# Performance work log

Measured on AMD Instinct MI355X. Metric: run time of the kernel, lower is better.

## Reference

```python
import jax, jax.numpy as jnp
import numpy as np

N, E, G = 40000, 640000, 32
H, HEADS, L, O = 128, 4, 4, 100
C = H // HEADS


def setup_inputs() -> dict:
    key = jax.random.key(0)
    ks = iter(jax.random.split(key, 40))
    def w(shape, fan):
        return jax.random.normal(next(ks), shape, jnp.float32) / np.float32(np.sqrt(fan))
    inp = {}
    inp["x"] = jax.random.normal(next(ks), (N, 4), jnp.float32)
    inp["edge_attr"] = jax.random.normal(next(ks), (E, 5), jnp.float32)
    inp["node_w"] = w((4, H), 4); inp["node_b"] = jnp.zeros((H,), jnp.float32)
    inp["edge_w"] = w((5, H), 5); inp["edge_b"] = jnp.zeros((H,), jnp.float32)
    inp["Wq"] = w((L, H, H), H); inp["bq"] = jnp.zeros((L, H), jnp.float32)
    inp["Wk"] = w((L, H, H), H); inp["bk"] = jnp.zeros((L, H), jnp.float32)
    inp["Wv"] = w((L, H, H), H); inp["bv"] = jnp.zeros((L, H), jnp.float32)
    inp["We"] = w((L, H, H), H)  # lin_edge has bias=False in PyG TransformerConv
    inp["Wskip"] = w((L, H, H), H); inp["bskip"] = jnp.zeros((L, H), jnp.float32)
    inp["ln_g"] = jnp.ones((L, H), jnp.float32); inp["ln_b"] = jnp.zeros((L, H), jnp.float32)
    inp["dos_w1"] = w((H, H // 2), H); inp["dos_b1"] = jnp.zeros((H // 2,), jnp.float32)
    inp["dos_w2"] = w((H // 2, O), H // 2); inp["dos_b2"] = jnp.zeros((O,), jnp.float32)
    inp["tr_w1"] = w((H, H // 2), H); inp["tr_b1"] = jnp.zeros((H // 2,), jnp.float32)
    inp["tr_w2"] = w((H // 2, O), H // 2); inp["tr_b2"] = jnp.zeros((O,), jnp.float32)
    inp["edge_index"] = jax.random.randint(next(ks), (2, E), 0, N, jnp.int32)
    inp["batch"] = jnp.sort(jax.random.randint(next(ks), (N,), 0, G, jnp.int32))
    return inp


def _seg_softmax(a, seg, n):
    # numerically stable scatter-softmax over edges grouped by destination node
    m = jax.ops.segment_max(a, seg, num_segments=n)
    e = jnp.exp(a - m[seg])
    s = jax.ops.segment_sum(e, seg, num_segments=n)
    return e / (s[seg] + 1e-16)


def _layer_norm(x, g, b, eps=1e-5):
    mu = x.mean(-1, keepdims=True)
    var = ((x - mu) ** 2).mean(-1, keepdims=True)
    return (x - mu) * jax.lax.rsqrt(var + eps) * g + b


def _forward(x, edge_attr, node_w, node_b, edge_w, edge_b, Wq, bq, Wk, bk, Wv, bv,
             We, Wskip, bskip, ln_g, ln_b,
             dos_w1, dos_b1, dos_w2, dos_b2, tr_w1, tr_b1, tr_w2, tr_b2,
             edge_index, batch):
    src, dst = edge_index[0], edge_index[1]  # PyG default flow: source->target
    n = x.shape[0]
    h = x @ node_w + node_b        # [N, H] node_proj
    e_h = edge_attr @ edge_w + edge_b  # [E, H] edge_proj (shared across layers)
    scale = np.float32(1.0 / np.sqrt(C))
    for i in range(L):  # TransformerConv -> LayerNorm -> ReLU (dropout is eval-mode no-op)
        q = (h @ Wq[i] + bq[i]).reshape(n, HEADS, C)
        k = (h @ Wk[i] + bk[i]).reshape(n, HEADS, C)
        v = (h @ Wv[i] + bv[i]).reshape(n, HEADS, C)
        e = (e_h @ We[i]).reshape(-1, HEADS, C)
        kj = k[src] + e            # [E, heads, C]
        vj = v[src] + e
        alpha = jnp.sum(q[dst] * kj, axis=-1) * scale  # [E, heads]
        alpha = _seg_softmax(alpha, dst, n)
        msg = vj * alpha[..., None]
        out = jax.ops.segment_sum(msg, dst, num_segments=n).reshape(n, H)
        out = out + h @ Wskip[i] + bskip[i]  # root_weight skip
        h = jax.nn.relu(_layer_norm(out, ln_g[i], ln_b[i]))
    # global mean pool per graph
    sums = jax.ops.segment_sum(h, batch, num_segments=G)
    cnt = jax.ops.segment_sum(jnp.ones((n, 1), h.dtype), batch, num_segments=G)
    hg = sums / jnp.maximum(cnt, 1.0)
    dos = jax.nn.relu(hg @ dos_w1 + dos_b1) @ dos_w2 + dos_b2
    tr = jax.nn.relu(hg @ tr_w1 + tr_b1) @ tr_w2 + tr_b2
    return dos, tr


def reference(x, edge_attr, node_w, node_b, edge_w, edge_b, Wq, bq, Wk, bk, Wv, bv,
              We, Wskip, bskip, ln_g, ln_b,
              dos_w1, dos_b1, dos_w2, dos_b2, tr_w1, tr_b1, tr_w2, tr_b2,
              edge_index, batch):
    return _forward(x, edge_attr, node_w, node_b, edge_w, edge_b, Wq, bq, Wk, bk, Wv, bv,
                    We, Wskip, bskip, ln_g, ln_b,
                    dos_w1, dos_b1, dos_w2, dos_b2, tr_w1, tr_b1, tr_w2, tr_b2,
                    edge_index, batch)
```

## Files before the change

kernel.cpp:

```cpp
#include <hip/hip_runtime.h>
#include <hip/hip_fp16.h>
#include <math.h>

#define N_NODES 40000
#define N_EDGES 640000
#define N_GRAPHS 32
#define HDIM 128
#define NHEADS 4
#define CDIM 32
#define NLAYERS 4
#define ODIM 100
#define SCAN_B 256
#define SCAN_NBLK ((N_NODES + SCAN_B - 1) / SCAN_B)
#define M_PAD 40064
#define POOL_CHUNK 32
#define POOL_NBLK ((N_NODES + POOL_CHUNK - 1) / POOL_CHUNK)
#define SCALE 0.17677669529663687f

typedef __bf16 bf16_t;
typedef bf16_t bf16x8 __attribute__((ext_vector_type(8)));
typedef float f32x4 __attribute__((ext_vector_type(4)));
typedef _Float16 h2v __attribute__((ext_vector_type(2)));

#if defined(__has_builtin)
#if __has_builtin(__builtin_amdgcn_fdot2)
#define HAVE_FDOT2 1
#endif
#endif

struct __align__(8) H2P { __half2 k; __half2 v; };

__global__ void nodeproj_kernel(const float* __restrict__ x,
                                const float* __restrict__ w,
                                const float* __restrict__ b,
                                bf16_t* __restrict__ hb) {
    int idx = blockIdx.x * blockDim.x + threadIdx.x;
    if (idx >= N_NODES * HDIM) return;
    int n = idx >> 7, c = idx & 127;
    float s = b[c];
    s += x[n * 4 + 0] * w[0 * HDIM + c];
    s += x[n * 4 + 1] * w[1 * HDIM + c];
    s += x[n * 4 + 2] * w[2 * HDIM + c];
    s += x[n * 4 + 3] * w[3 * HDIM + c];
    hb[idx] = (bf16_t)s;
}

__global__ void fold_edge_kernel(const float* __restrict__ edge_w,
                                 const float* __restrict__ edge_b,
                                 const float* __restrict__ We,
                                 float* __restrict__ Me_all,
                                 float* __restrict__ ce_all) {
    int blk = blockIdx.x;
    int i = blk / 6, j = blk % 6;
    int c = threadIdx.x;
    const float* W = We + (size_t)i * HDIM * HDIM;
    float s = 0.0f;
    if (j < 5) {
        for (int k = 0; k < HDIM; ++k) s += edge_w[j * HDIM + k] * W[k * HDIM + c];
        Me_all[i * 5 * HDIM + j * HDIM + c] = s;
    } else {
        for (int k = 0; k < HDIM; ++k) s += edge_b[k] * W[k * HDIM + c];
        ce_all[i * HDIM + c] = s;
    }
}

__global__ void count_deg_kernel(const int* __restrict__ ei, int* __restrict__ deg) {
    int e = blockIdx.x * blockDim.x + threadIdx.x;
    if (e >= N_EDGES) return;
    atomicAdd(&deg[ei[N_EDGES + e]], 1);
}

__global__ void scan1_kernel(const int* __restrict__ deg,
                             int* __restrict__ rowptr, int* __restrict__ bsum) {
    __shared__ int sd[SCAN_B];
    int tid = threadIdx.x;
    int i = blockIdx.x * SCAN_B + tid;
    int v = (i < N_NODES) ? deg[i] : 0;
    sd[tid] = v;
    __syncthreads();
#pragma unroll
    for (int off = 1; off < SCAN_B; off <<= 1) {
        int tmp = (tid >= off) ? sd[tid - off] : 0;
        __syncthreads();
        sd[tid] += tmp;
        __syncthreads();
    }
    if (i < N_NODES) rowptr[i] = sd[tid] - v;
    if (tid == SCAN_B - 1) bsum[blockIdx.x] = sd[tid];
}

__global__ void scan2_kernel(const int* __restrict__ bsum, int* __restrict__ bscan) {
    __shared__ int sd[SCAN_B];
    int tid = threadIdx.x;
    int v = (tid < SCAN_NBLK) ? bsum[tid] : 0;
    sd[tid] = v;
    __syncthreads();
#pragma unroll
    for (int off = 1; off < SCAN_B; off <<= 1) {
        int tmp = (tid >= off) ? sd[tid - off] : 0;
        __syncthreads();
        sd[tid] += tmp;
        __syncthreads();
    }
    if (tid < SCAN_NBLK) bscan[tid] = sd[tid] - v;
}

__global__ void scan3_kernel(int* __restrict__ rowptr, const int* __restrict__ bscan) {
    int i = blockIdx.x * SCAN_B + threadIdx.x;
    if (i < N_NODES) rowptr[i] += bscan[blockIdx.x];
    if (i == 0) rowptr[N_NODES] = N_EDGES;
}

__global__ void fill_csr_kernel(const int* __restrict__ ei,
                                const float* __restrict__ ea,
                                const int* __restrict__ rowptr,
                                int* __restrict__ cursor,
                                int* __restrict__ srcarr,
                                float* __restrict__ ea8) {
    int e = blockIdx.x * blockDim.x + threadIdx.x;
    if (e >= N_EDGES) return;
    int src = ei[e], dst = ei[N_EDGES + e];
    int pos = atomicAdd(&cursor[dst], 1);
    int p = rowptr[dst] + pos;
    srcarr[p] = src;
    float4 lo = make_float4(ea[(size_t)e * 5 + 0], ea[(size_t)e * 5 + 1],
                            ea[(size_t)e * 5 + 2], ea[(size_t)e * 5 + 3]);
    float4 hi = make_float4(ea[(size_t)e * 5 + 4], 0.f, 0.f, 0.f);
    *(float4*)(ea8 + (size_t)p * 8)     = lo;
    *(float4*)(ea8 + (size_t)p * 8 + 4) = hi;
}

__global__ void convert_w_kernel(const float* __restrict__ Wq, const float* __restrict__ Wk,
                                 const float* __restrict__ Wv, const float* __restrict__ Ws,
                                 bf16_t* __restrict__ Wtb) {
    int b = blockIdx.x;
    int n = b & 127;
    int matli = b >> 7;
    int mat = matli & 3, li = matli >> 2;
    int kk = threadIdx.x;
    const float* W = (mat == 0 ? Wq : mat == 1 ? Wk : mat == 2 ? Wv : Ws) + (size_t)li * HDIM * HDIM;
    float val = W[kk * HDIM + n];
    if (mat == 1) val *= SCALE;
    Wtb[((size_t)(li * 4 + mat) * HDIM + n) * HDIM + kk] = (bf16_t)val;
}

__global__ __launch_bounds__(256) void gemm_mfma(
    const bf16_t* __restrict__ hb, const bf16_t* __restrict__ Wt,
    const float* __restrict__ bq, const float* __restrict__ bk,
    const float* __restrict__ bv, const float* __restrict__ bs,
    __half2* __restrict__ q2o, H2P* __restrict__ kv2o,
    float* __restrict__ so) {
    __shared__ bf16_t Ash[128 * 128];
    __shared__ bf16_t Bsh[128 * 128];
    int tid = threadIdx.x;
    int mt = blockIdx.y;
    int row0 = blockIdx.x * 128;
    int r = tid >> 4, g = tid & 15;

    {
        const bf16_t* W0 = Wt + (size_t)(mt == 0 ? 0 : (mt == 1 ? 1 : 3)) * HDIM * HDIM;
#pragma unroll
        for (int p = 0; p < 8; ++p) {
            int rr = p * 16 + r;
            int sw = (g ^ (rr & 15)) << 3;
            *(bf16x8*)(Ash + rr * 128 + sw) = *(const bf16x8*)(hb + (size_t)(row0 + rr) * HDIM + g * 8);
            *(bf16x8*)(Bsh + rr * 128 + sw) = *(const bf16x8*)(W0 + (size_t)rr * HDIM + g * 8);
        }
    }
    __syncthreads();

    int lane = tid & 63, wave = tid >> 6;
    int wr = (wave >> 1) * 64, wc = (wave & 1) * 64;
    int lm = lane & 15, quad = lane >> 4;

    f32x4 acc[4][4];
#pragma unroll
    for (int i = 0; i < 4; ++i)
#pragma unroll
        for (int j = 0; j < 4; ++j) acc[i][j] = (f32x4){0.f, 0.f, 0.f, 0.f};

#pragma unroll
    for (int ks = 0; ks < 4; ++ks) {
        int gg = ks * 4 + quad;
        int sw = (gg ^ lm) << 3;
        bf16x8 af[4], bf[4];
#pragma unroll
        for (int t = 0; t < 4; ++t) {
            af[t] = *(const bf16x8*)(Ash + (wr + t * 16 + lm) * 128 + sw);
            bf[t] = *(const bf16x8*)(Bsh + (wc + t * 16 + lm) * 128 + sw);
        }
#pragma unroll
        for (int i = 0; i < 4; ++i)
#pragma unroll
            for (int j = 0; j < 4; ++j)
                acc[i][j] = __builtin_amdgcn_mfma_f32_16x16x32_bf16(af[i], bf[j], acc[i][j], 0, 0, 0);
    }

    int c0 = wc + lm;
    int c2 = wc + lm + 32;
    int pi0 = ((c0 >> 5) << 4) | lm;
    int pi1 = ((c2 >> 5) << 4) | lm;

    if (mt == 0) {
        float b0 = bq[c0], b1 = bq[c0 + 16], b2 = bq[c2], b3 = bq[c2 + 16];
#pragma unroll
        for (int i = 0; i < 4; ++i) {
            int rbase = row0 + wr + i * 16 + quad * 4;
#pragma unroll
            for (int rr2 = 0; rr2 < 4; ++rr2) {
                int row = rbase + rr2;
                if (row < N_NODES) {
                    q2o[(size_t)row * 64 + pi0] =
                        __floats2half2_rn(acc[i][0][rr2] + b0, acc[i][1][rr2] + b1);
                    q2o[(size_t)row * 64 + pi1] =
                        __floats2half2_rn(acc[i][2][rr2] + b2, acc[i][3][rr2] + b3);
                }
            }
        }
    } else if (mt == 1) {
        f32x4 acc2[4][4];
#pragma unroll
        for (int i = 0; i < 4; ++i)
#pragma unroll
            for (int j = 0; j < 4; ++j) acc2[i][j] = (f32x4){0.f, 0.f, 0.f, 0.f};
        __syncthreads();
        {
            const bf16_t* W1 = Wt + (size_t)2 * HDIM * HDIM;
#pragma unroll
            for (int p = 0; p < 8; ++p) {
                int rr = p * 16 + r;
                int sw = (g ^ (rr & 15)) << 3;
                *(bf16x8*)(Bsh + rr * 128 + sw) = *(const bf16x8*)(W1 + (size_t)rr * HDIM + g * 8);
            }
        }
        __syncthreads();
#pragma unroll
        for (int ks = 0; ks < 4; ++ks) {
            int gg = ks * 4 + quad;
            int sw = (gg ^ lm) << 3;
            bf16x8 af[4], bf[4];
#pragma unroll
            for (int t = 0; t < 4; ++t) {
                af[t] = *(const bf16x8*)(Ash + (wr + t * 16 + lm) * 128 + sw);
                bf[t] = *(const bf16x8*)(Bsh + (wc + t * 16 + lm) * 128 + sw);
            }
#pragma unroll
            for (int i = 0; i < 4; ++i)
#pragma unroll
                for (int j = 0; j < 4; ++j)
                    acc2[i][j] = __builtin_amdgcn_mfma_f32_16x16x32_bf16(af[i], bf[j], acc2[i][j], 0, 0, 0);
        }
        float kb0 = bk[c0] * SCALE, kb1 = bk[c0 + 16] * SCALE;
        float kb2 = bk[c2] * SCALE, kb3 = bk[c2 + 16] * SCALE;
        float vb0 = bv[c0], vb1 = bv[c0 + 16], vb2 = bv[c2], vb3 = bv[c2 + 16];
#pragma unroll
        for (int i = 0; i < 4; ++i) {
            int rbase = row0 + wr + i * 16 + quad * 4;
#pragma unroll
            for (int rr2 = 0; rr2 < 4; ++rr2) {
                int row = rbase + rr2;
                if (row < N_NODES) {
                    H2P h0, h1;
                    h0.k = __floats2half2_rn(acc[i][0][rr2] + kb0, acc[i][1][rr2] + kb1);
                    h0.v = __floats2half2_rn(acc2[i][0][rr2] + vb0, acc2[i][1][rr2] + vb1);
                    h1.k = __floats2half2_rn(acc[i][2][rr2] + kb2, acc[i][3][rr2] + kb3);
                    h1.v = __floats2half2_rn(acc2[i][2][rr2] + vb2, acc2[i][3][rr2] + vb3);
                    kv2o[(size_t)row * 64 + pi0] = h0;
                    kv2o[(size_t)row * 64 + pi1] = h1;
                }
            }
        }
    } else {
#pragma unroll
        for (int i = 0; i < 4; ++i) {
            int rbase = row0 + wr + i * 16 + quad * 4;
#pragma unroll
            for (int j = 0; j < 4; ++j) {
                int col = wc + j * 16 + lm;
                float bcol = bs[col];
#pragma unroll
                for (int rr2 = 0; rr2 < 4; ++rr2) {
                    int row = rbase + rr2;
                    if (row < N_NODES) so[(size_t)row * HDIM + col] = acc[i][j][rr2] + bcol;
                }
            }
        }
    }
}

__global__ __launch_bounds__(128) void agg_kernel(
    const int* __restrict__ srcarr, const int* __restrict__ rowptr,
    const float* __restrict__ ea8,
    const __half2* __restrict__ q2,
    const H2P* __restrict__ kv2,
    const float* __restrict__ Me, const float* __restrict__ ce,
    const float* __restrict__ skip,
    const float* __restrict__ lg, const float* __restrict__ lb,
    bf16_t* __restrict__ hbout) {
    int t = threadIdx.x & 63;
    int n = blockIdx.x * 2 + (threadIdx.x >> 6);
    int cc = t & 15;
    int clo = ((t >> 4) << 5) | cc;
    int chi = clo + 16;

    __half2 qh = q2[(size_t)n * 64 + t];
    float2 qf = __half22float2(qh);
    float cwlo = ce[clo], cwhi = ce[chi];
    float mlo[5], mhi[5];
#pragma unroll
    for (int j = 0; j < 5; ++j) { mlo[j] = Me[j * HDIM + clo]; mhi[j] = Me[j * HDIM + chi]; }

    float myq = 0.0f;
#pragma unroll
    for (int j = 0; j < 6; ++j) {
        float a = (j < 5) ? mlo[j] : cwlo;
        float b = (j < 5) ? mhi[j] : cwhi;
        float p = (qf.x * a + qf.y * b) * SCALE;
        p += __shfl_xor(p, 8, 16);
        p += __shfl_xor(p, 4, 16);
        p += __shfl_xor(p, 2, 16);
        p += __shfl_xor(p, 1, 16);
        if (cc == j) myq = p;
    }

    int beg = rowptr[n], end = rowptr[n + 1];
    float l[4], o0[4], o1[4], ab[4];
#pragma unroll
    for (int s = 0; s < 4; ++s) { l[s] = 0.f; o0[s] = 0.f; o1[s] = 0.f; ab[s] = 0.f; }

    if (beg < end) {
        int e1 = end - 1;
        int srcB[4];
        float avA[4], avB[4];
        H2P kvA[4];
        {
            int srcA[4];
#pragma unroll
            for (int s = 0; s < 4; ++s) {
                int ca = beg + s;       ca = (ca < e1) ? ca : e1;
                int cb = beg + 4 + s;   cb = (cb < e1) ? cb : e1;
                srcA[s] = srcarr[ca];
                srcB[s] = srcarr[cb];
                avA[s] = (cc < 5) ? ea8[(size_t)ca * 8 + cc] : 1.0f;
                avB[s] = (cc < 5) ? ea8[(size_t)cb * 8 + cc] : 1.0f;
            }
#pragma unroll
            for (int s = 0; s < 4; ++s) kvA[s] = kv2[(size_t)srcA[s] * 64 + t];
        }

        for (int base = beg; base < end; base += 4) {
            H2P kvB[4];
#pragma unroll
            for (int s = 0; s < 4; ++s) kvB[s] = kv2[(size_t)srcB[s] * 64 + t];
            int srcC[4]; float avC[4];
#pragma unroll
            for (int s = 0; s < 4; ++s) {
                int cidx = base + 8 + s; cidx = (cidx < e1) ? cidx : e1;
                srcC[s] = srcarr[cidx];
                avC[s] = (cc < 5) ? ea8[(size_t)cidx * 8 + cc] : 1.0f;
            }
            float p4[4], vx[4], vy[4];
#pragma unroll
            for (int s = 0; s < 4; ++s) {
                float2 vf = __half22float2(kvA[s].v);
                vx[s] = vf.x; vy[s] = vf.y;
                float pa = myq * avA[s];
#if defined(HAVE_FDOT2)
                p4[s] = __builtin_amdgcn_fdot2(__builtin_bit_cast(h2v, qh),
                                               __builtin_bit_cast(h2v, kvA[s].k), pa, false);
#else
                float2 kf = __half22float2(kvA[s].k);
                p4[s] = fmaf(qf.x, kf.x, fmaf(qf.y, kf.y, pa));
#endif
            }
#pragma unroll
            for (int st = 8; st >= 1; st >>= 1) {
#pragma unroll
                for (int s = 0; s < 4; ++s) p4[s] += __shfl_xor(p4[s], st, 16);
            }
#pragma unroll
            for (int s = 0; s < 4; ++s) {
                float pe = (base + s < end) ? __expf(p4[s]) : 0.0f;
                o0[s] = fmaf(pe, vx[s], o0[s]);
                o1[s] = fmaf(pe, vy[s], o1[s]);
                l[s] += pe;
                ab[s] = fmaf(pe, avA[s], ab[s]);
            }
#pragma unroll
            for (int s = 0; s < 4; ++s) {
                kvA[s] = kvB[s];
                avA[s] = avB[s];
                srcB[s] = srcC[s];
                avB[s] = avC[s];
            }
        }
    }
    float lt  = (l[0] + l[1]) + (l[2] + l[3]);
    float o0t = (o0[0] + o0[1]) + (o0[2] + o0[3]);
    float o1t = (o1[0] + o1[1]) + (o1[2] + o1[3]);
    float abt = (ab[0] + ab[1]) + (ab[2] + ab[3]);

    float nlo = fmaf(lt, cwlo, o0t);
    float nhi = fmaf(lt, cwhi, o1t);
#pragma unroll
    for (int j = 0; j < 5; ++j) {
        float abj = __shfl(abt, (t & 48) + j, 64);
        nlo = fmaf(mlo[j], abj, nlo);
        nhi = fmaf(mhi[j], abj, nhi);
    }
    float inv = 1.0f / (lt + 1e-16f);
    float vlo = skip[(size_t)n * HDIM + clo] + nlo * inv;
    float vhi = skip[(size_t)n * HDIM + chi] + nhi * inv;

    float s = vlo + vhi;
#pragma unroll
    for (int mask = 32; mask >= 1; mask >>= 1) s += __shfl_xor(s, mask, 64);
    float mu = s * (1.0f / HDIM);
    float dlo = vlo - mu, dhi = vhi - mu;
    float s2 = dlo * dlo + dhi * dhi;
#pragma unroll
    for (int mask = 32; mask >= 1; mask >>= 1) s2 += __shfl_xor(s2, mask, 64);
    float rstd = rsqrtf(s2 * (1.0f / HDIM) + 1e-5f);
    float ylo = fmaxf(dlo * rstd * lg[clo] + lb[clo], 0.0f);
    float yhi = fmaxf(dhi * rstd * lg[chi] + lb[chi], 0.0f);
    hbout[(size_t)n * HDIM + clo] = (bf16_t)ylo;
    hbout[(size_t)n * HDIM + chi] = (bf16_t)yhi;
}

__global__ __launch_bounds__(128) void pool_kernel(const bf16_t* __restrict__ h,
                                                   const int* __restrict__ batch,
                                                   float* __restrict__ pool,
                                                   float* __restrict__ cnt) {
    int t = threadIdx.x;
    int n0 = blockIdx.x * POOL_CHUNK;
    int n1 = n0 + POOL_CHUNK;
    if (n1 > N_NODES) n1 = N_NODES;
    int gcur = batch[n0];
    int cstart = n0;
    float acc = 0.0f;
    for (int n = n0; n < n1; ++n) {
        int g = batch[n];
        if (g != gcur) {
            atomicAdd(&pool[gcur * HDIM + t], acc);
            if (t == 0) atomicAdd(&cnt[gcur], (float)(n - cstart));
            acc = 0.0f;
            gcur = g;
            cstart = n;
        }
        acc += (float)h[(size_t)n * HDIM + t];
    }
    atomicAdd(&pool[gcur * HDIM + t], acc);
    if (t == 0) atomicAdd(&cnt[gcur], (float)(n1 - cstart));
}

__global__ void heads_kernel(const float* __restrict__ pool,
                             const float* __restrict__ cnt,
                             const float* __restrict__ dw1, const float* __restrict__ db1,
                             const float* __restrict__ dw2, const float* __restrict__ db2,
                             const float* __restrict__ tw1, const float* __restrict__ tb1,
                             const float* __restrict__ tw2, const float* __restrict__ tb2,
                             float* __restrict__ outp) {
    int g = blockIdx.x, t = threadIdx.x;
    __shared__ float hg[HDIM];
    __shared__ float hid[64];
    float c = fmaxf(cnt[g], 1.0f);
    hg[t] = pool[g * HDIM + t] / c;
    __syncthreads();
    if (t < 64) {
        float s = db1[t];
        for (int i = 0; i < HDIM; ++i) s += hg[i] * dw1[i * 64 + t];
        hid[t] = fmaxf(s, 0.0f);
    }
    __syncthreads();
    if (t < ODIM) {
        float s = db2[t];
        for (int j = 0; j < 64; ++j) s += hid[j] * dw2[j * ODIM + t];
        outp[g * ODIM + t] = s;
    }
    __syncthreads();
    if (t < 64) {
        float s = tb1[t];
        for (int i = 0; i < HDIM; ++i) s += hg[i] * tw1[i * 64 + t];
        hid[t] = fmaxf(s, 0.0f);
    }
    __syncthreads();
    if (t < ODIM) {
        float s = tb2[t];
        for (int j = 0; j < 64; ++j) s += hid[j] * tw2[j * ODIM + t];
        outp[N_GRAPHS * ODIM + g * ODIM + t] = s;
    }
}

extern "C" void kernel_launch(void* const* d_in, const int* in_sizes, int n_in,
                              void* d_out, int out_size, void* d_ws, size_t ws_size,
                              hipStream_t stream) {
    const float* x        = (const float*)d_in[0];
    const float* ea       = (const float*)d_in[1];
    const float* node_w   = (const float*)d_in[2];
    const float* node_b   = (const float*)d_in[3];
    const float* edge_w   = (const float*)d_in[4];
    const float* edge_b   = (const float*)d_in[5];
    const float* Wq       = (const float*)d_in[6];
    const float* bq       = (const float*)d_in[7];
    const float* Wk       = (const float*)d_in[8];
    const float* bk       = (const float*)d_in[9];
    const float* Wv       = (const float*)d_in[10];
    const float* bv       = (const float*)d_in[11];
    const float* We       = (const float*)d_in[12];
    const float* Wskip    = (const float*)d_in[13];
    const float* bskip    = (const float*)d_in[14];
    const float* ln_g     = (const float*)d_in[15];
    const float* ln_b     = (const float*)d_in[16];
    const float* dw1      = (const float*)d_in[17];
    const float* db1      = (const float*)d_in[18];
    const float* dw2      = (const float*)d_in[19];
    const float* db2      = (const float*)d_in[20];
    const float* tw1      = (const float*)d_in[21];
    const float* tb1      = (const float*)d_in[22];
    const float* tw2      = (const float*)d_in[23];
    const float* tb2      = (const float*)d_in[24];
    const int*   ei       = (const int*)d_in[25];
    const int*   batch    = (const int*)d_in[26];
    float* out = (float*)d_out;
    (void)in_sizes; (void)n_in; (void)out_size; (void)ws_size;

    char* wsb = (char*)d_ws;
    size_t off = 0;
    auto carve = [&](size_t bytes) -> void* {
        void* p = wsb + off;
        off += (bytes + 255) & ~(size_t)255;
        return p;
    };
    bf16_t*  hbuf   = (bf16_t*) carve((size_t)M_PAD * HDIM * 2);
    __half2* q2b    = (__half2*)carve((size_t)N_NODES * 64 * 4);
    H2P*     kv2b   = (H2P*)    carve((size_t)N_NODES * 64 * 8);
    float*   ob     = (float*)  carve((size_t)N_NODES * HDIM * 4);
    bf16_t*  Wtb    = (bf16_t*) carve((size_t)NLAYERS * 4 * HDIM * HDIM * 2);
    int*     srcarr = (int*)    carve((size_t)N_EDGES * 4);
    float*   ea8    = (float*)  carve((size_t)N_EDGES * 8 * 4);
    int*     deg    = (int*)    carve((size_t)N_NODES * 4);
    int*     cursor = (int*)    carve((size_t)N_NODES * 4);
    int*     rowptr = (int*)    carve((size_t)(N_NODES + 1) * 4);
    int*     bsum   = (int*)    carve((size_t)SCAN_NBLK * 4);
    int*     bscan  = (int*)    carve((size_t)SCAN_NBLK * 4);
    float*   Me_all = (float*)  carve((size_t)NLAYERS * 5 * HDIM * 4);
    float*   ce_all = (float*)  carve((size_t)NLAYERS * HDIM * 4);
    float*   pool   = (float*)  carve((size_t)N_GRAPHS * HDIM * 4);
    float*   cnt    = (float*)  carve((size_t)N_GRAPHS * 4);

    const int nthreads = 256;
    const int e_blocks  = (N_EDGES + nthreads - 1) / nthreads;
    const int nc_blocks = (N_NODES * HDIM) / nthreads;

    hipMemsetAsync(deg, 0, (size_t)N_NODES * 4 * 2, stream);
    count_deg_kernel<<<e_blocks, nthreads, 0, stream>>>(ei, deg);
    scan1_kernel<<<SCAN_NBLK, SCAN_B, 0, stream>>>(deg, rowptr, bsum);
    scan2_kernel<<<1, SCAN_B, 0, stream>>>(bsum, bscan);
    scan3_kernel<<<SCAN_NBLK, SCAN_B, 0, stream>>>(rowptr, bscan);
    fill_csr_kernel<<<e_blocks, nthreads, 0, stream>>>(ei, ea, rowptr, cursor, srcarr, ea8);

    hipMemsetAsync(hbuf + (size_t)N_NODES * HDIM, 0,
                   (size_t)(M_PAD - N_NODES) * HDIM * 2, stream);
    nodeproj_kernel<<<nc_blocks, nthreads, 0, stream>>>(x, node_w, node_b, hbuf);
    fold_edge_kernel<<<NLAYERS * 6, HDIM, 0, stream>>>(edge_w, edge_b, We, Me_all, ce_all);
    convert_w_kernel<<<NLAYERS * 4 * HDIM, HDIM, 0, stream>>>(Wq, Wk, Wv, Wskip, Wtb);

    for (int i = 0; i < NLAYERS; ++i) {
        const float* Me = Me_all + i * 5 * HDIM;
        const float* ce = ce_all + i * HDIM;
        gemm_mfma<<<dim3(M_PAD / 128, 3), 256, 0, stream>>>(
            hbuf, Wtb + (size_t)i * 4 * HDIM * HDIM,
            bq + i * HDIM, bk + i * HDIM, bv + i * HDIM, bskip + i * HDIM,
            q2b, kv2b, ob);
        agg_kernel<<<N_NODES / 2, 128, 0, stream>>>(srcarr, rowptr, ea8, q2b, kv2b,
                                                    Me, ce, ob,
                                                    ln_g + i * HDIM, ln_b + i * HDIM, hbuf);
    }

    hipMemsetAsync(pool, 0, (size_t)(N_GRAPHS * HDIM + N_GRAPHS) * 4, stream);
    pool_kernel<<<POOL_NBLK, HDIM, 0, stream>>>(hbuf, batch, pool, cnt);
    heads_kernel<<<N_GRAPHS, HDIM, 0, stream>>>(pool, cnt, dw1, db1, dw2, db2,
                                                tw1, tb1, tw2, tb2, out);
}
```

Measured before the change: 563.4 us.

## Double GEMM block to 512 threads with eight waves each owning 64x32 tiles

```diff
diff --git a/kernel.cpp b/kernel.cpp
--- a/kernel.cpp
+++ b/kernel.cpp
@@ -144,7 +144,7 @@
     Wtb[((size_t)(li * 4 + mat) * HDIM + n) * HDIM + kk] = (bf16_t)val;
 }
 
-__global__ __launch_bounds__(256) void gemm_mfma(
+__global__ __launch_bounds__(512) void gemm_mfma(
     const bf16_t* __restrict__ hb, const bf16_t* __restrict__ Wt,
     const float* __restrict__ bq, const float* __restrict__ bk,
     const float* __restrict__ bv, const float* __restrict__ bs,
@@ -155,13 +155,13 @@
     int tid = threadIdx.x;
     int mt = blockIdx.y;
     int row0 = blockIdx.x * 128;
-    int r = tid >> 4, g = tid & 15;
 
     {
         const bf16_t* W0 = Wt + (size_t)(mt == 0 ? 0 : (mt == 1 ? 1 : 3)) * HDIM * HDIM;
 #pragma unroll
-        for (int p = 0; p < 8; ++p) {
-            int rr = p * 16 + r;
+        for (int p = 0; p < 4; ++p) {
+            int i = tid + p * 512;
+            int rr = i >> 4, g = i & 15;
             int sw = (g ^ (rr & 15)) << 3;
             *(bf16x8*)(Ash + rr * 128 + sw) = *(const bf16x8*)(hb + (size_t)(row0 + rr) * HDIM + g * 8);
             *(bf16x8*)(Bsh + rr * 128 + sw) = *(const bf16x8*)(W0 + (size_t)rr * HDIM + g * 8);
@@ -170,65 +170,62 @@
     __syncthreads();
 
     int lane = tid & 63, wave = tid >> 6;
-    int wr = (wave >> 1) * 64, wc = (wave & 1) * 64;
+    int wr = (wave >> 2) * 64, wc = (wave & 3) * 32;
     int lm = lane & 15, quad = lane >> 4;
 
-    f32x4 acc[4][4];
+    f32x4 acc[4][2];
 #pragma unroll
     for (int i = 0; i < 4; ++i)
 #pragma unroll
-        for (int j = 0; j < 4; ++j) acc[i][j] = (f32x4){0.f, 0.f, 0.f, 0.f};
+        for (int j = 0; j < 2; ++j) acc[i][j] = (f32x4){0.f, 0.f, 0.f, 0.f};
 
 #pragma unroll
     for (int ks = 0; ks < 4; ++ks) {
         int gg = ks * 4 + quad;
         int sw = (gg ^ lm) << 3;
-        bf16x8 af[4], bf[4];
-#pragma unroll
-        for (int t = 0; t < 4; ++t) {
+        bf16x8 af[4], bf[2];
+#pragma unroll
+        for (int t = 0; t < 4; ++t)
             af[t] = *(const bf16x8*)(Ash + (wr + t * 16 + lm) * 128 + sw);
-            bf[t] = *(const bf16x8*)(Bsh + (wc + t * 16 + lm) * 128 + sw);
-        }
+#pragma unroll
+        for (int j = 0; j < 2; ++j)
+            bf[j] = *(const bf16x8*)(Bsh + (wc + j * 16 + lm) * 128 + sw);
 #pragma unroll
         for (int i = 0; i < 4; ++i)
 #pragma unroll
-            for (int j = 0; j < 4; ++j)
+            for (int j = 0; j < 2; ++j)
                 acc[i][j] = __builtin_amdgcn_mfma_f32_16x16x32_bf16(af[i], bf[j], acc[i][j], 0, 0, 0);
     }
 
     int c0 = wc + lm;
-    int c2 = wc + lm + 32;
-    int pi0 = ((c0 >> 5) << 4) | lm;
-    int pi1 = ((c2 >> 5) << 4) | lm;
+    int pi = ((wave & 3) << 4) | lm;
 
     if (mt == 0) {
-        float b0 = bq[c0], b1 = bq[c0 + 16], b2 = bq[c2], b3 = bq[c2 + 16];
+        float b0 = bq[c0], b1 = bq[c0 + 16];
 #pragma unroll
         for (int i = 0; i < 4; ++i) {
             int rbase = row0 + wr + i * 16 + quad * 4;
 #pragma unroll
-            for (int rr2 = 0; rr2 < 4; ++rr2) {
-                int row = rbase + rr2;
-                if (row < N_NODES) {
-                    q2o[(size_t)row * 64 + pi0] =
-                        __floats2half2_rn(acc[i][0][rr2] + b0, acc[i][1][rr2] + b1);
-                    q2o[(size_t)row * 64 + pi1] =
-                        __floats2half2_rn(acc[i][2][rr2] + b2, acc[i][3][rr2] + b3);
-                }
+            for (int r = 0; r < 4; ++r) {
+                int row = rbase + r;
+                if (row < N_NODES)
+                    q2o[(size_t)row * 64 + pi] =
+                        __floats2half2_rn(acc[i][0][r] + b0, acc[i][1][r] + b1);
             }
         }
     } else if (mt == 1) {
-        f32x4 acc2[4][4];
+        f32x4 acc2[4][2];
 #pragma unroll
         for (int i = 0; i < 4; ++i)
 #pragma unroll
-            for (int j = 0; j < 4; ++j) acc2[i][j] = (f32x4){0.f, 0.f, 0.f, 0.f};
+            for (int j = 0; j < 2; ++j) acc2[i][j] = (f32x4){0.f, 0.f, 0.f, 0.f};
         __syncthreads();
         {
             const bf16_t* W1 = Wt + (size_t)2 * HDIM * HDIM;
 #pragma unroll
-            for (int p = 0; p < 8; ++p) {
-                int rr = p * 16 + r;
+            for (int p = 0; p < 4; ++p) {
+                int i = tid + p * 512;
+                int rr = i >> 4, g = i & 15;
                 int sw = (g ^ (rr & 15)) << 3;
                 *(bf16x8*)(Bsh + rr * 128 + sw) = *(const bf16x8*)(W1 + (size_t)rr * HDIM + g * 8);
             }
@@ -238,50 +235,46 @@
         for (int ks = 0; ks < 4; ++ks) {
             int gg = ks * 4 + quad;
             int sw = (gg ^ lm) << 3;
-            bf16x8 af[4], bf[4];
-#pragma unroll
-            for (int t = 0; t < 4; ++t) {
+            bf16x8 af[4], bf[2];
+#pragma unroll
+            for (int t = 0; t < 4; ++t)
                 af[t] = *(const bf16x8*)(Ash + (wr + t * 16 + lm) * 128 + sw);
-                bf[t] = *(const bf16x8*)(Bsh + (wc + t * 16 + lm) * 128 + sw);
-            }
+#pragma unroll
+            for (int j = 0; j < 2; ++j)
+                bf[j] = *(const bf16x8*)(Bsh + (wc + j * 16 + lm) * 128 + sw);
 #pragma unroll
             for (int i = 0; i < 4; ++i)
 #pragma unroll
-                for (int j = 0; j < 4; ++j)
+                for (int j = 0; j < 2; ++j)
                     acc2[i][j] = __builtin_amdgcn_mfma_f32_16x16x32_bf16(af[i], bf[j], acc2[i][j], 0, 0, 0);
         }
         float kb0 = bk[c0] * SCALE, kb1 = bk[c0 + 16] * SCALE;
-        float kb2 = bk[c2] * SCALE, kb3 = bk[c2 + 16] * SCALE;
-        float vb0 = bv[c0], vb1 = bv[c0 + 16], vb2 = bv[c2], vb3 = bv[c2 + 16];
+        float vb0 = bv[c0], vb1 = bv[c0 + 16];
 #pragma unroll
         for (int i = 0; i < 4; ++i) {
             int rbase = row0 + wr + i * 16 + quad * 4;
 #pragma unroll
-            for (int rr2 = 0; rr2 < 4; ++rr2) {
-                int row = rbase + rr2;
+            for (int r = 0; r < 4; ++r) {
+                int row = rbase + r;
                 if (row < N_NODES) {
-                    H2P h0, h1;
-                    h0.k = __floats2half2_rn(acc[i][0][rr2] + kb0, acc[i][1][rr2] + kb1);
-                    h0.v = __floats2half2_rn(acc2[i][0][rr2] + vb0, acc2[i][1][rr2] + vb1);
-                    h1.k = __floats2half2_rn(acc[i][2][rr2] + kb2, acc[i][3][rr2] + kb3);
-                    h1.v = __floats2half2_rn(acc2[i][2][rr2] + vb2, acc2[i][3][rr2] + vb3);
-                    kv2o[(size_t)row * 64 + pi0] = h0;
-                    kv2o[(size_t)row * 64 + pi1] = h1;
+                    H2P h;
+                    h.k = __floats2half2_rn(acc[i][0][r] + kb0, acc[i][1][r] + kb1);
+                    h.v = __floats2half2_rn(acc2[i][0][r] + vb0, acc2[i][1][r] + vb1);
+                    kv2o[(size_t)row * 64 + pi] = h;
                 }
             }
         }
     } else {
+        float b0 = bs[c0], b1 = bs[c0 + 16];
 #pragma unroll
         for (int i = 0; i < 4; ++i) {
             int rbase = row0 + wr + i * 16 + quad * 4;
 #pragma unroll
-            for (int j = 0; j < 4; ++j) {
-                int col = wc + j * 16 + lm;
-                float bcol = bs[col];
-#pragma unroll
-                for (int rr2 = 0; rr2 < 4; ++rr2) {
-                    int row = rbase + rr2;
-                    if (row < N_NODES) so[(size_t)row * HDIM + col] = acc[i][j][rr2] + bcol;
+            for (int r = 0; r < 4; ++r) {
+                int row = rbase + r;
+                if (row < N_NODES) {
+                    so[(size_t)row * HDIM + c0]      = acc[i][0][r] + b0;
+                    so[(size_t)row * HDIM + c0 + 16] = acc[i][1][r] + b1;
                 }
             }
         }
@@ -568,7 +561,7 @@
     for (int i = 0; i < NLAYERS; ++i) {
         const float* Me = Me_all + i * 5 * HDIM;
         const float* ce = ce_all + i * HDIM;
-        gemm_mfma<<<dim3(M_PAD / 128, 3), 256, 0, stream>>>(
+        gemm_mfma<<<dim3(M_PAD / 128, 3), 512, 0, stream>>>(
             hbuf, Wtb + (size_t)i * 4 * HDIM * HDIM,
             bq + i * HDIM, bk + i * HDIM, bv + i * HDIM, bskip + i * HDIM,
             q2b, kv2b, ob);
```

Measured after the change: 546.3 us, median of 2. 1.03x faster.
